# Performance work log

Hardware: AMD Instinct MI355X
Metric: run time of the kernel (lower is better)

Reference implementation:

```python
import jax, jax.numpy as jnp
import numpy as np

B, C, H, W = 8, 256, 32, 32
DK, HEADS = 64, 4
DQ = DK * HEADS            # lambda attention: query dim = dim_key * num_heads
DV = 256 // HEADS          # out_channels // num_heads
EPS = 1e-5
SF = DK ** (-0.25)


def setup_inputs() -> dict:
    key = jax.random.key(0)
    ks = jax.random.split(key, 6)
    inv = 1.0 / np.sqrt(C)
    return {
        "input": jax.random.normal(ks[0], (B, C, H, W), jnp.float32),
        "Wq": jax.random.normal(ks[1], (DQ, C), jnp.float32) * inv,
        "gamma_q": jnp.ones((DQ,), jnp.float32),
        "beta_q": jnp.zeros((DQ,), jnp.float32),
        "Wk": jax.random.normal(ks[2], (DK, C), jnp.float32) * inv,
        "gamma_k": jnp.ones((DK,), jnp.float32),
        "beta_k": jnp.zeros((DK,), jnp.float32),
        "Wv": jax.random.normal(ks[3], (DV, C), jnp.float32) * inv,
        "rpe": jax.random.normal(ks[4], (2 * max(H, W) - 1, 2 * max(H, W) - 1, DK), jnp.float32),
    }


def _bn(x, gamma, beta):
    # BatchNorm2d in training mode: batch stats over (B, H, W), biased variance
    mu = jnp.mean(x, axis=(0, 2, 3), keepdims=True)
    var = jnp.var(x, axis=(0, 2, 3), keepdims=True)
    xn = (x - mu) * jax.lax.rsqrt(var + EPS)
    return xn * gamma[None, :, None, None] + beta[None, :, None, None]


def reference(input, Wq, gamma_q, beta_q, Wk, gamma_k, beta_k, Wv, rpe):
    b, c, h, w = input.shape
    n = h * w
    size = max(h, w)

    # conv1x1 projections (no bias)
    q = _bn(jnp.einsum('oc,bchw->bohw', Wq, input), gamma_q, beta_q)
    k = _bn(jnp.einsum('oc,bchw->bohw', Wk, input), gamma_k, beta_k)
    v = jnp.einsum('oc,bchw->bohw', Wv, input)

    q = q.reshape(b, HEADS, DK, n) * SF          # [b,h,k,n]
    k = k.reshape(b, DK, n) * SF                 # single kv head -> [b,k,n]
    v = v.reshape(b, DV, n)                      # [b,v,n]

    # lambda attention: content lambda
    ks = jax.nn.softmax(k, axis=-1)
    context = jnp.einsum('bkn,bvn->bkv', ks, v)
    out = jnp.einsum('bkv,bhkn->bhvn', context, q)

    # positional lambda via relative position embedding gather
    pos = jnp.arange(size)
    grid = jnp.stack(jnp.meshgrid(pos, pos, indexing='ij'), axis=-1).reshape(-1, 2)  # [n,2]
    rel = grid[None, :] - grid[:, None] + (size - 1)                                 # [n,n,2]
    rg = rpe[rel[..., 0], rel[..., 1]]                                               # [n,n,k]
    pos_context = jnp.einsum('nmk,bvm->bnkv', rg, v)
    out = out + jnp.einsum('bhkn,bnkv->bhvn', q, pos_context)

    return out.reshape(b, -1, h, w)
```

## Files before the change

### kernel.cpp

```cpp
#include <hip/hip_runtime.h>

#define SFC 0.35355339059327373f

typedef __attribute__((ext_vector_type(8))) short short8;
typedef __attribute__((ext_vector_type(16))) float f32x16;
typedef unsigned short ushort_t;

__device__ __forceinline__ float4 ld4(const float* p) { return *reinterpret_cast<const float4*>(p); }
__device__ __forceinline__ void st4(float* p, float4 v) { *reinterpret_cast<float4*>(p) = v; }

union F4 { float4 v; float f[4]; };
union S8 { short8 v; ushort_t u[8]; };

__device__ __forceinline__ ushort_t bfb(float f) {
  union { float f; unsigned u; } a; a.f = f;
  unsigned r = a.u + 0x7FFFu + ((a.u >> 16) & 1u);
  return (ushort_t)(r >> 16);
}

__device__ __forceinline__ void gl16(const void* g, void* l) {
  __builtin_amdgcn_global_load_lds(
      (const __attribute__((address_space(1))) unsigned int*)g,
      (__attribute__((address_space(3))) unsigned int*)l, 16, 0, 0);
}

__global__ __launch_bounds__(256) void k_prep(
    const float* __restrict__ rpe, const float* __restrict__ wq,
    const float* __restrict__ wk, const float* __restrict__ wv,
    const float* __restrict__ x, ushort_t* __restrict__ RPEB2,
    ushort_t* __restrict__ WB, ushort_t* __restrict__ XBT)
{
  const int bx = blockIdx.x, t = threadIdx.x;
  if (bx < 63) {
    const int di = bx;
#pragma unroll
    for (int it = 0; it < 2; ++it) {
      const int slot = t + it * 256;
      const int tkc = slot >> 6;
      const int l = slot & 63, lnp = l & 31, hip = l >> 5;
      const int dj = (tkc >> 2) * 32 + lnp;
      const int k = (tkc & 3) * 16 + hip * 8;
      S8 o;
      if (dj < 63) {
        const float* s = rpe + (size_t)di * 4032 + dj * 64 + k;
        float4 a = ld4(s), b = ld4(s + 4);
        o.u[0] = bfb(a.x); o.u[1] = bfb(a.y); o.u[2] = bfb(a.z); o.u[3] = bfb(a.w);
        o.u[4] = bfb(b.x); o.u[5] = bfb(b.y); o.u[6] = bfb(b.z); o.u[7] = bfb(b.w);
      } else {
#pragma unroll
        for (int i = 0; i < 8; ++i) o.u[i] = 0;
      }
      *(short8*)(RPEB2 + (size_t)di * 4096 + tkc * 512 + l * 8) = o.v;
    }
  } else if (bx < 111) {
    const int cc = (bx - 63) * 256 + t;
    const int o = cc >> 5, k8 = (cc & 31) * 8;
    const float* src = (o < 256) ? (wq + o * 256)
                      : (o < 320) ? (wk + (o - 256) * 256)
                                  : (wv + (o - 320) * 256);
    float4 a = ld4(src + k8), b = ld4(src + k8 + 4);
    S8 s;
    s.u[0] = bfb(a.x); s.u[1] = bfb(a.y); s.u[2] = bfb(a.z); s.u[3] = bfb(a.w);
    s.u[4] = bfb(b.x); s.u[5] = bfb(b.y); s.u[6] = bfb(b.z); s.u[7] = bfb(b.w);
    *(short8*)(WB + (size_t)o * 256 + k8) = s.v;
  } else {
    const int id = (bx - 111) * 256 + t;
    const int ng = id & 8191, c8 = id >> 13;
    const int bb = ng >> 10, nn = ng & 1023;
    const float* src = x + (size_t)bb * 262144 + (size_t)(c8 * 8) * 1024 + nn;
    S8 s;
#pragma unroll
    for (int j = 0; j < 8; ++j) s.u[j] = bfb(src[(size_t)j * 1024]);
    *(short8*)(XBT + (size_t)ng * 256 + c8 * 8) = s.v;
  }
}

__global__ __launch_bounds__(256) void k_projm(
    const ushort_t* __restrict__ WB, const ushort_t* __restrict__ XBT,
    float* __restrict__ P, ushort_t* __restrict__ VB2,
    float* __restrict__ PSUM, float* __restrict__ PSQ)
{
  __shared__ ushort_t At[64 * 72];
  __shared__ ushort_t Bt[128 * 72];
  const int t = threadIdx.x;
  const int bm = blockIdx.x, bn = blockIdx.y;
  const int o0 = bm * 64, col0 = bn * 128;
  const int w = t >> 6, l = t & 63, ln = l & 31, hi = l >> 5;
  const int wm = w & 1, wn = w >> 1;

  f32x16 acc0, acc1;
#pragma unroll
  for (int i = 0; i < 16; ++i) { acc0[i] = 0.f; acc1[i] = 0.f; }

  for (int k0 = 0; k0 < 256; k0 += 64) {
    __syncthreads();
#pragma unroll
    for (int i = 0; i < 2; ++i) {
      const int c = t + i * 256, row = c >> 3, k8 = (c & 7) * 8;
      *(short8*)(At + row * 72 + k8) =
          *(const short8*)(WB + (size_t)(o0 + row) * 256 + k0 + k8);
    }
#pragma unroll
    for (int i = 0; i < 4; ++i) {
      const int c = t + i * 256, row = c >> 3, k8 = (c & 7) * 8;
      *(short8*)(Bt + row * 72 + k8) =
          *(const short8*)(XBT + (size_t)(col0 + row) * 256 + k0 + k8);
    }
    __syncthreads();
    const ushort_t* ka  = At + (wm * 32 + ln) * 72 + hi * 8;
    const ushort_t* kb0 = Bt + (wn * 64 + ln) * 72 + hi * 8;
    const ushort_t* kb1 = Bt + (wn * 64 + 32 + ln) * 72 + hi * 8;
#pragma unroll
    for (int kc = 0; kc < 4; ++kc) {
      short8 a = *(const short8*)(ka + kc * 16);
      acc0 = __builtin_amdgcn_mfma_f32_32x32x16_bf16(a, *(const short8*)(kb0 + kc * 16), acc0, 0, 0, 0);
      acc1 = __builtin_amdgcn_mfma_f32_32x32x16_bf16(a, *(const short8*)(kb1 + kc * 16), acc1, 0, 0, 0);
    }
  }

#pragma unroll
  for (int r = 0; r < 16; ++r) {
    const int o = o0 + wm * 32 + (r & 3) + 8 * (r >> 2) + 4 * hi;
    float* dst = P + (size_t)o * 8192 + col0 + wn * 64 + ln;
    dst[0]  = acc0[r];
    dst[32] = acc1[r];
  }
  if (bm == 5) {
    const int b2 = bn >> 3;
    const int n0 = (bn & 7) * 128 + wn * 64 + ln;
#pragma unroll
    for (int r = 0; r < 16; ++r) {
      const int v = wm * 32 + (r & 3) + 8 * (r >> 2) + 4 * hi;
#pragma unroll
      for (int half = 0; half < 2; ++half) {
        const int n = n0 + half * 32;
        const int i2 = n >> 5, j2 = n & 31;
        const float val = half ? acc1[r] : acc0[r];
        VB2[(((size_t)(b2 * 32 + i2) * 2 + wm) * 2 + (j2 >> 4)) * 512
            + ((v & 31) + 32 * ((j2 >> 3) & 1)) * 8 + (j2 & 7)] = bfb(val);
      }
    }
  } else {
#pragma unroll
    for (int r = 0; r < 16; ++r) {
      float s1 = acc0[r] + acc1[r];
      float s2 = acc0[r] * acc0[r] + acc1[r] * acc1[r];
#pragma unroll
      for (int off = 1; off < 32; off <<= 1) {
        s1 += __shfl_xor(s1, off, 64);
        s2 += __shfl_xor(s2, off, 64);
      }
      if (ln == 0) {
        const int o = o0 + wm * 32 + (r & 3) + 8 * (r >> 2) + 4 * hi;
        PSUM[o * 128 + bn * 2 + wn] = s1;
        PSQ [o * 128 + bn * 2 + wn] = s2;
      }
    }
  }
}

__global__ __launch_bounds__(128) void k_bnfin(
    const float* __restrict__ PSUM, const float* __restrict__ PSQ,
    const float* __restrict__ gq, const float* __restrict__ bq,
    const float* __restrict__ gk, const float* __restrict__ bk,
    float* __restrict__ scale, float* __restrict__ shift)
{
  const int ch = blockIdx.x, t = threadIdx.x;
  float s1 = PSUM[ch * 128 + t];
  float s2 = PSQ[ch * 128 + t];
#pragma unroll
  for (int off = 1; off < 64; off <<= 1) {
    s1 += __shfl_xor(s1, off, 64);
    s2 += __shfl_xor(s2, off, 64);
  }
  __shared__ float red[4];
  if ((t & 63) == 0) { red[t >> 6] = s1; red[2 + (t >> 6)] = s2; }
  __syncthreads();
  if (t == 0) {
    s1 = red[0] + red[1];
    s2 = red[2] + red[3];
    const float mu = s1 * (1.0f / 8192.0f);
    const float var = s2 * (1.0f / 8192.0f) - mu * mu;
    const float rsig = rsqrtf(var + 1e-5f);
    float g, be;
    if (ch < 256) { g = gq[ch]; be = bq[ch]; }
    else          { g = gk[ch - 256]; be = bk[ch - 256]; }
    const float sc = rsig * g * SFC;
    scale[ch] = sc;
    shift[ch] = be * SFC - mu * sc;
  }
}

__global__ __launch_bounds__(256) void k_softmax(
    const float* __restrict__ P, const float* __restrict__ scale,
    const float* __restrict__ shift, ushort_t* __restrict__ KSB)
{
  const int b = blockIdx.x >> 6, kc = blockIdx.x & 63;
  const int ch = 256 + kc;
  const float sc = scale[ch], sh = shift[ch];
  const float4* row = (const float4*)(P + (size_t)ch * 8192 + b * 1024);
  float4 v = row[threadIdx.x];
  float y0 = v.x * sc + sh, y1 = v.y * sc + sh;
  float y2 = v.z * sc + sh, y3 = v.w * sc + sh;
  float m = fmaxf(fmaxf(y0, y1), fmaxf(y2, y3));
#pragma unroll
  for (int off = 32; off; off >>= 1) m = fmaxf(m, __shfl_xor(m, off, 64));
  __shared__ float red[8];
  const int w = threadIdx.x >> 6, lane = threadIdx.x & 63;
  if (lane == 0) red[w] = m;
  __syncthreads();
  m = fmaxf(fmaxf(red[0], red[1]), fmaxf(red[2], red[3]));
  const float e0 = __expf(y0 - m), e1 = __expf(y1 - m);
  const float e2 = __expf(y2 - m), e3 = __expf(y3 - m);
  float su = e0 + e1 + e2 + e3;
#pragma unroll
  for (int off = 32; off; off >>= 1) su += __shfl_xor(su, off, 64);
  if (lane == 0) red[4 + w] = su;
  __syncthreads();
  const float inv = 1.0f / (red[4] + red[5] + red[6] + red[7]);
  ushort4 u;
  u.x = bfb(e0 * inv); u.y = bfb(e1 * inv);
  u.z = bfb(e2 * inv); u.w = bfb(e3 * inv);
  ((ushort4*)(KSB + (size_t)(b * 64 + kc) * 1024))[threadIdx.x] = u;
}

__global__ __launch_bounds__(256) void k_ctxm(
    const ushort_t* __restrict__ KSB, const ushort_t* __restrict__ VB2,
    ushort_t* __restrict__ CTXB)
{
  __shared__ ushort_t KT[2][64 * 72];
  const int b = blockIdx.x, t = threadIdx.x;
  const int w = t >> 6, l = t & 63, ln = l & 31, hi = l >> 5;
  const int a = w & 1, bt = w >> 1;

  auto stageK = [&](int ch, int buf) {
    const int n0 = ch * 64;
#pragma unroll
    for (int it = 0; it < 2; ++it) {
      const int idx = t + it * 256;
      const int row = idx >> 3, seg = idx & 7;
      *(short8*)(&KT[buf][row * 72 + seg * 8]) =
          *(const short8*)(KSB + (size_t)(b * 64 + row) * 1024 + n0 + seg * 8);
    }
  };

  f32x16 acc;
#pragma unroll
  for (int i = 0; i < 16; ++i) acc[i] = 0.f;

  stageK(0, 0);
  for (int ch = 0; ch < 16; ++ch) {
    const int cur = ch & 1;
    __syncthreads();
    if (ch + 1 < 16) stageK(ch + 1, cur ^ 1);
    const ushort_t* ka = &KT[cur][(a * 32 + ln) * 72 + hi * 8];
#pragma unroll
    for (int cc = 0; cc < 4; ++cc) {
      const int i2 = ch * 2 + (cc >> 1), c = cc & 1;
      short8 bf = *(const short8*)(VB2 +
          (((size_t)(b * 32 + i2) * 2 + bt) * 2 + c) * 512 + l * 8);
      acc = __builtin_amdgcn_mfma_f32_32x32x16_bf16(
          *(const short8*)(ka + cc * 16), bf, acc, 0, 0, 0);
    }
  }
#pragma unroll
  for (int r = 0; r < 16; ++r) {
    const int kc = a * 32 + (r & 3) + 8 * (r >> 2) + 4 * hi;
    CTXB[(size_t)b * 4608 + (bt * 32 + ln) * 72 + kc] = bfb(acc[r]);
  }
}

extern __shared__ char ldsc[];

__global__ __launch_bounds__(512) void k_pos(
    const float* __restrict__ P, const ushort_t* __restrict__ RPEB2,
    const ushort_t* __restrict__ VB2, const float* __restrict__ scale,
    const float* __restrict__ shift, const ushort_t* __restrict__ CTXB,
    float* __restrict__ out)
{
  float* qst = (float*)ldsc;
  ushort_t* SlB = (ushort_t*)(ldsc + 33792);
  char* CtxL = ldsc + 54272;

  const int t = threadIdx.x;
  const int b = blockIdx.x >> 5, i1 = blockIdx.x & 31;
  const int w = t >> 6, l = t & 63, ln = l & 31, hi = l >> 5;
  const int m = w & 3, g = w >> 2;

  {
    const char* cs = (const char*)CTXB + (size_t)b * 9216;
    gl16(cs + w * 1024 + l * 16, CtxL + w * 1024 + l * 16);
    if (w == 0) gl16(cs + 8192 + l * 16, CtxL + 8192 + l * 16);
  }

  const ushort_t* rbase = RPEB2 + (size_t)(g * 16 - i1 + 31) * 4096;
  const ushort_t* vbase = VB2 + (size_t)(b * 32 + g * 16) * 2048;

  short8 rA[8], rB[8];
#pragma unroll
  for (int f = 0; f < 8; ++f) rA[f] = *(const short8*)(rbase + f * 512 + l * 8);

  {
    const int j1 = t & 31, c0 = (t >> 5) * 16;
    const float* src = P + (size_t)b * 1024 + i1 * 32 + j1;
#pragma unroll
    for (int i = 0; i < 16; ++i) {
      const int ch = c0 + i;
      qst[ch * 33 + j1] = src[(size_t)ch * 8192] * scale[ch] + shift[ch];
    }
  }
  __syncthreads();

  short8 qf[4];
#pragma unroll
  for (int kc = 0; kc < 4; ++kc) {
    S8 s;
#pragma unroll
    for (int i = 0; i < 8; ++i)
      s.u[i] = bfb(qst[(m * 64 + kc * 16 + hi * 8 + i) * 33 + ln]);
    qf[kc] = s.v;
  }

  f32x16 sv0, sv1;
#pragma unroll
  for (int i = 0; i < 16; ++i) { sv0[i] = 0.f; sv1[i] = 0.f; }

  ushort_t* sm = SlB + w * 1280;

  auto body = [&](int s, const short8* R) {
    const ushort_t* vp = vbase + (size_t)s * 2048 + l * 8;
    short8 v00 = *(const short8*)(vp);
    short8 v01 = *(const short8*)(vp + 512);
    short8 v10 = *(const short8*)(vp + 1024);
    short8 v11 = *(const short8*)(vp + 1536);
    f32x16 t0, t1;
#pragma unroll
    for (int i = 0; i < 16; ++i) { t0[i] = 0.f; t1[i] = 0.f; }
#pragma unroll
    for (int kc = 0; kc < 4; ++kc) {
      t0 = __builtin_amdgcn_mfma_f32_32x32x16_bf16(qf[kc], R[kc],     t0, 0, 0, 0);
      t1 = __builtin_amdgcn_mfma_f32_32x32x16_bf16(qf[kc], R[4 + kc], t1, 0, 0, 0);
    }
#pragma unroll
    for (int r = 0; r < 16; ++r) {
      const int j1 = (r & 3) + 8 * (r >> 2) + 4 * hi;
      const int j2a = ln + j1 - 31;
      const int j2b = 32 + ln + j1 - 31;
      if ((unsigned)j2a < 32u) sm[j1 * 40 + j2a] = bfb(t0[r]);
      if ((unsigned)j2b < 32u) sm[j1 * 40 + j2b] = bfb(t1[r]);
    }
    const ushort_t* sa = sm + ln * 40 + hi * 8;
    short8 sA0 = *(const short8*)(sa);
    short8 sA1 = *(const short8*)(sa + 16);
    sv0 = __builtin_amdgcn_mfma_f32_32x32x16_bf16(sA0, v00, sv0, 0, 0, 0);
    sv0 = __builtin_amdgcn_mfma_f32_32x32x16_bf16(sA1, v01, sv0, 0, 0, 0);
    sv1 = __builtin_amdgcn_mfma_f32_32x32x16_bf16(sA0, v10, sv1, 0, 0, 0);
    sv1 = __builtin_amdgcn_mfma_f32_32x32x16_bf16(sA1, v11, sv1, 0, 0, 0);
  };

  for (int s = 0; s < 16; s += 2) {
    {
      const ushort_t* rn = rbase + (size_t)(s + 1) * 4096;
#pragma unroll
      for (int f = 0; f < 8; ++f) rB[f] = *(const short8*)(rn + f * 512 + l * 8);
    }
    body(s, rA);
    if (s + 2 < 16) {
      const ushort_t* rn = rbase + (size_t)(s + 2) * 4096;
#pragma unroll
      for (int f = 0; f < 8; ++f) rA[f] = *(const short8*)(rn + f * 512 + l * 8);
    }
    body(s + 1, rB);
  }

  __syncthreads();

  float* out_l = qst;
  if (g == 0) {
    const ushort_t* cb = (const ushort_t*)CtxL;
    const ushort_t* c0 = cb + ln * 72 + hi * 8;
    const ushort_t* c1 = cb + (32 + ln) * 72 + hi * 8;
#pragma unroll
    for (int kc = 0; kc < 4; ++kc) {
      sv0 = __builtin_amdgcn_mfma_f32_32x32x16_bf16(qf[kc], *(const short8*)(c0 + kc * 16), sv0, 0, 0, 0);
      sv1 = __builtin_amdgcn_mfma_f32_32x32x16_bf16(qf[kc], *(const short8*)(c1 + kc * 16), sv1, 0, 0, 0);
    }
  } else {
#pragma unroll
    for (int r = 0; r < 16; ++r) {
      const int j1 = (r & 3) + 8 * (r >> 2) + 4 * hi;
      out_l[(m * 64 + ln) * 33 + j1]      = sv0[r];
      out_l[(m * 64 + 32 + ln) * 33 + j1] = sv1[r];
    }
  }
  __syncthreads();
  if (g == 0) {
#pragma unroll
    for (int r = 0; r < 16; ++r) {
      const int j1 = (r & 3) + 8 * (r >> 2) + 4 * hi;
      out_l[(m * 64 + ln) * 33 + j1]      += sv0[r];
      out_l[(m * 64 + 32 + ln) * 33 + j1] += sv1[r];
    }
  }
  __syncthreads();
  {
    const int ch = t >> 1, jh = (t & 1) * 16;
    float* dst = out + (size_t)b * 262144 + (size_t)ch * 1024 + i1 * 32 + jh;
    const float* srow = out_l + ch * 33 + jh;
#pragma unroll
    for (int gq2 = 0; gq2 < 4; ++gq2)
      st4(dst + gq2 * 4, make_float4(srow[gq2 * 4], srow[gq2 * 4 + 1],
                                     srow[gq2 * 4 + 2], srow[gq2 * 4 + 3]));
  }
}

extern "C" void kernel_launch(void* const* d_in, const int* in_sizes, int n_in,
                              void* d_out, int out_size, void* d_ws, size_t ws_size,
                              hipStream_t stream) {
  const float* x   = (const float*)d_in[0];
  const float* wq  = (const float*)d_in[1];
  const float* gq  = (const float*)d_in[2];
  const float* bq  = (const float*)d_in[3];
  const float* wk  = (const float*)d_in[4];
  const float* gk  = (const float*)d_in[5];
  const float* bk  = (const float*)d_in[6];
  const float* wv  = (const float*)d_in[7];
  const float* rpe = (const float*)d_in[8];
  float* out = (float*)d_out;
  char* W = (char*)d_ws;

  float* P        = (float*)W;
  ushort_t* KSB   = (ushort_t*)(W + 12582912);
  float* PSUM     = (float*)(W + 13631488);
  float* PSQ      = (float*)(W + 13795328);
  float* SCALE    = (float*)(W + 13959168);
  float* SHIFT    = (float*)(W + 13961216);
  ushort_t* CTXB  = (ushort_t*)(W + 13963264);
  ushort_t* RPEB2 = (ushort_t*)(W + 14036992);
  ushort_t* VB2   = (ushort_t*)(W + 14553088);
  ushort_t* WB    = (ushort_t*)(W + 15601664);
  ushort_t* XBT   = (ushort_t*)(W + 15798272);

  k_prep<<<1135, 256, 0, stream>>>(rpe, wq, wk, wv, x, RPEB2, WB, XBT);
  k_projm<<<dim3(6, 64), 256, 0, stream>>>(WB, XBT, P, VB2, PSUM, PSQ);
  k_bnfin<<<320, 128, 0, stream>>>(PSUM, PSQ, gq, bq, gk, bk, SCALE, SHIFT);
  k_softmax<<<512, 256, 0, stream>>>(P, SCALE, SHIFT, KSB);
  k_ctxm<<<8, 256, 0, stream>>>(KSB, VB2, CTXB);

  hipFuncSetAttribute((const void*)k_pos,
                      hipFuncAttributeMaxDynamicSharedMemorySize, 63488);
  k_pos<<<256, 512, 63488, stream>>>(P, RPEB2, VB2, SCALE, SHIFT, CTXB, out);
}
```

Baseline: 62.01 us.

## Store Q as bf16 in MFMA fragment layout, fuse BN finalize into softmax

The projection kernel now writes Q directly as bf16 in the fragment layout k_pos consumes, and keeps only K in fp32. This replaces the full fp32 P buffer with a smaller one and removes the LDS staging and transpose of Q in k_pos. The separate BN-finalize kernel is folded into k_softmax: extra blocks compute the Q scale and shift, while each K block recomputes its own channel stats, which removes one launch. Q is now rounded to bf16 before normalization and rounded again after, which adds a little precision loss.

After: 59.41 us. -4.2%, faster.

```diff
diff --git a/kernel.cpp b/kernel.cpp
--- a/kernel.cpp
+++ b/kernel.cpp
@@ -16,6 +16,9 @@
   union { float f; unsigned u; } a; a.f = f;
   unsigned r = a.u + 0x7FFFu + ((a.u >> 16) & 1u);
   return (ushort_t)(r >> 16);
+}
+__device__ __forceinline__ float bf2f(ushort_t u) {
+  union { unsigned u; float f; } a; a.u = (unsigned)u << 16; return a.f;
 }
 
 __device__ __forceinline__ void gl16(const void* g, void* l) {
@@ -77,8 +80,9 @@
 
 __global__ __launch_bounds__(256) void k_projm(
     const ushort_t* __restrict__ WB, const ushort_t* __restrict__ XBT,
-    float* __restrict__ P, ushort_t* __restrict__ VB2,
-    float* __restrict__ PSUM, float* __restrict__ PSQ)
+    float* __restrict__ Pk, ushort_t* __restrict__ QB,
+    ushort_t* __restrict__ VB2, float* __restrict__ PSUM,
+    float* __restrict__ PSQ)
 {
   __shared__ ushort_t At[64 * 72];
   __shared__ ushort_t Bt[128 * 72];
@@ -118,13 +122,6 @@
     }
   }
 
-#pragma unroll
-  for (int r = 0; r < 16; ++r) {
-    const int o = o0 + wm * 32 + (r & 3) + 8 * (r >> 2) + 4 * hi;
-    float* dst = P + (size_t)o * 8192 + col0 + wn * 64 + ln;
-    dst[0]  = acc0[r];
-    dst[32] = acc1[r];
-  }
   if (bm == 5) {
     const int b2 = bn >> 3;
     const int n0 = (bn & 7) * 128 + wn * 64 + ln;
@@ -141,6 +138,31 @@
       }
     }
   } else {
+    if (bm == 4) {
+#pragma unroll
+      for (int r = 0; r < 16; ++r) {
+        const int o = o0 + wm * 32 + (r & 3) + 8 * (r >> 2) + 4 * hi;
+        float* dst = Pk + (size_t)(o - 256) * 8192 + col0 + wn * 64 + ln;
+        dst[0]  = acc0[r];
+        dst[32] = acc1[r];
+      }
+    } else {
+      const int kcq = 2 * wm;
+#pragma unroll
+      for (int r = 0; r < 16; ++r) {
+        const int kc = kcq + ((r >> 3) & 1);
+        const int lq = ln + 32 * ((r >> 2) & 1);
+        const int iq = (r & 3) + 4 * hi;
+#pragma unroll
+        for (int half = 0; half < 2; ++half) {
+          const int n = col0 + wn * 64 + half * 32 + ln;
+          const int bq_ = n >> 10, i1q = (n >> 5) & 31;
+          const float val = half ? acc1[r] : acc0[r];
+          QB[(((size_t)(bq_ * 32 + i1q) * 4 + bm) * 4 + kc) * 512 + lq * 8 + iq] =
+              bfb(val);
+        }
+      }
+    }
 #pragma unroll
     for (int r = 0; r < 16; ++r) {
       float s1 = acc0[r] + acc1[r];
@@ -159,69 +181,89 @@
   }
 }
 
-__global__ __launch_bounds__(128) void k_bnfin(
-    const float* __restrict__ PSUM, const float* __restrict__ PSQ,
-    const float* __restrict__ gq, const float* __restrict__ bq,
-    const float* __restrict__ gk, const float* __restrict__ bk,
-    float* __restrict__ scale, float* __restrict__ shift)
+__global__ __launch_bounds__(256) void k_softmax(
+    const float* __restrict__ Pk, const float* __restrict__ PSUM,
+    const float* __restrict__ PSQ, const float* __restrict__ gq,
+    const float* __restrict__ bq, const float* __restrict__ gk,
+    const float* __restrict__ bk, float* __restrict__ SCALE,
+    float* __restrict__ SHIFT, ushort_t* __restrict__ KSB)
 {
-  const int ch = blockIdx.x, t = threadIdx.x;
-  float s1 = PSUM[ch * 128 + t];
-  float s2 = PSQ[ch * 128 + t];
-#pragma unroll
-  for (int off = 1; off < 64; off <<= 1) {
-    s1 += __shfl_xor(s1, off, 64);
-    s2 += __shfl_xor(s2, off, 64);
-  }
-  __shared__ float red[4];
-  if ((t & 63) == 0) { red[t >> 6] = s1; red[2 + (t >> 6)] = s2; }
-  __syncthreads();
-  if (t == 0) {
-    s1 = red[0] + red[1];
-    s2 = red[2] + red[3];
-    const float mu = s1 * (1.0f / 8192.0f);
-    const float var = s2 * (1.0f / 8192.0f) - mu * mu;
-    const float rsig = rsqrtf(var + 1e-5f);
-    float g, be;
-    if (ch < 256) { g = gq[ch]; be = bq[ch]; }
-    else          { g = gk[ch - 256]; be = bk[ch - 256]; }
-    const float sc = rsig * g * SFC;
-    scale[ch] = sc;
-    shift[ch] = be * SFC - mu * sc;
-  }
-}
-
-__global__ __launch_bounds__(256) void k_softmax(
-    const float* __restrict__ P, const float* __restrict__ scale,
-    const float* __restrict__ shift, ushort_t* __restrict__ KSB)
-{
+  __shared__ float red[8];
+  __shared__ float scsh[2];
+  const int t = threadIdx.x;
+
+  if (blockIdx.x >= 512) {
+    const int ch = blockIdx.x - 512;
+    float s1 = 0.f, s2 = 0.f;
+    if (t < 128) { s1 = PSUM[ch * 128 + t]; s2 = PSQ[ch * 128 + t]; }
+#pragma unroll
+    for (int off = 1; off < 64; off <<= 1) {
+      s1 += __shfl_xor(s1, off, 64);
+      s2 += __shfl_xor(s2, off, 64);
+    }
+    if ((t & 63) == 0) { red[t >> 6] = s1; red[4 + (t >> 6)] = s2; }
+    __syncthreads();
+    if (t == 0) {
+      s1 = red[0] + red[1] + red[2] + red[3];
+      s2 = red[4] + red[5] + red[6] + red[7];
+      const float mu = s1 * (1.0f / 8192.0f);
+      const float var = s2 * (1.0f / 8192.0f) - mu * mu;
+      const float sc = rsqrtf(var + 1e-5f) * gq[ch] * SFC;
+      SCALE[ch] = sc;
+      SHIFT[ch] = bq[ch] * SFC - mu * sc;
+    }
+    return;
+  }
+
   const int b = blockIdx.x >> 6, kc = blockIdx.x & 63;
-  const int ch = 256 + kc;
-  const float sc = scale[ch], sh = shift[ch];
-  const float4* row = (const float4*)(P + (size_t)ch * 8192 + b * 1024);
-  float4 v = row[threadIdx.x];
+  {
+    const int ch = 256 + kc;
+    float s1 = 0.f, s2 = 0.f;
+    if (t < 128) { s1 = PSUM[ch * 128 + t]; s2 = PSQ[ch * 128 + t]; }
+#pragma unroll
+    for (int off = 1; off < 64; off <<= 1) {
+      s1 += __shfl_xor(s1, off, 64);
+      s2 += __shfl_xor(s2, off, 64);
+    }
+    if ((t & 63) == 0) { red[t >> 6] = s1; red[4 + (t >> 6)] = s2; }
+    __syncthreads();
+    if (t == 0) {
+      s1 = red[0] + red[1] + red[2] + red[3];
+      s2 = red[4] + red[5] + red[6] + red[7];
+      const float mu = s1 * (1.0f / 8192.0f);
+      const float var = s2 * (1.0f / 8192.0f) - mu * mu;
+      const float sc = rsqrtf(var + 1e-5f) * gk[kc] * SFC;
+      scsh[0] = sc;
+      scsh[1] = bk[kc] * SFC - mu * sc;
+    }
+    __syncthreads();
+  }
+  const float sc = scsh[0], sh = scsh[1];
+
+  const float4* row = (const float4*)(Pk + (size_t)kc * 8192 + b * 1024);
+  float4 v = row[t];
   float y0 = v.x * sc + sh, y1 = v.y * sc + sh;
   float y2 = v.z * sc + sh, y3 = v.w * sc + sh;
   float m = fmaxf(fmaxf(y0, y1), fmaxf(y2, y3));
 #pragma unroll
   for (int off = 32; off; off >>= 1) m = fmaxf(m, __shfl_xor(m, off, 64));
-  __shared__ float red[8];
-  const int w = threadIdx.x >> 6, lane = threadIdx.x & 63;
-  if (lane == 0) red[w] = m;
+  __shared__ float red2[8];
+  const int w = t >> 6, lane = t & 63;
+  if (lane == 0) red2[w] = m;
   __syncthreads();
-  m = fmaxf(fmaxf(red[0], red[1]), fmaxf(red[2], red[3]));
+  m = fmaxf(fmaxf(red2[0], red2[1]), fmaxf(red2[2], red2[3]));
   const float e0 = __expf(y0 - m), e1 = __expf(y1 - m);
   const float e2 = __expf(y2 - m), e3 = __expf(y3 - m);
   float su = e0 + e1 + e2 + e3;
 #pragma unroll
   for (int off = 32; off; off >>= 1) su += __shfl_xor(su, off, 64);
-  if (lane == 0) red[4 + w] = su;
+  if (lane == 0) red2[4 + w] = su;
   __syncthreads();
-  const float inv = 1.0f / (red[4] + red[5] + red[6] + red[7]);
+  const float inv = 1.0f / (red2[4] + red2[5] + red2[6] + red2[7]);
   ushort4 u;
   u.x = bfb(e0 * inv); u.y = bfb(e1 * inv);
   u.z = bfb(e2 * inv); u.w = bfb(e3 * inv);
-  ((ushort4*)(KSB + (size_t)(b * 64 + kc) * 1024))[threadIdx.x] = u;
+  ((ushort4*)(KSB + (size_t)(b * 64 + kc) * 1024))[t] = u;
 }
 
 __global__ __launch_bounds__(256) void k_ctxm(
@@ -273,12 +315,12 @@
 extern __shared__ char ldsc[];
 
 __global__ __launch_bounds__(512) void k_pos(
-    const float* __restrict__ P, const ushort_t* __restrict__ RPEB2,
-    const ushort_t* __restrict__ VB2, const float* __restrict__ scale,
-    const float* __restrict__ shift, const ushort_t* __restrict__ CTXB,
+    const ushort_t* __restrict__ QB, const ushort_t* __restrict__ RPEB2,
+    const ushort_t* __restrict__ VB2, const float* __restrict__ SCALE,
+    const float* __restrict__ SHIFT, const ushort_t* __restrict__ CTXB,
     float* __restrict__ out)
 {
-  float* qst = (float*)ldsc;
+  float* out_l = (float*)ldsc;
   ushort_t* SlB = (ushort_t*)(ldsc + 33792);
   char* CtxL = ldsc + 54272;
 
@@ -300,25 +342,26 @@
 #pragma unroll
   for (int f = 0; f < 8; ++f) rA[f] = *(const short8*)(rbase + f * 512 + l * 8);
 
+  short8 qf[4];
   {
-    const int j1 = t & 31, c0 = (t >> 5) * 16;
-    const float* src = P + (size_t)b * 1024 + i1 * 32 + j1;
-#pragma unroll
-    for (int i = 0; i < 16; ++i) {
-      const int ch = c0 + i;
-      qst[ch * 33 + j1] = src[(size_t)ch * 8192] * scale[ch] + shift[ch];
-    }
-  }
-  __syncthreads();
-
-  short8 qf[4];
-#pragma unroll
-  for (int kc = 0; kc < 4; ++kc) {
-    S8 s;
-#pragma unroll
-    for (int i = 0; i < 8; ++i)
-      s.u[i] = bfb(qst[(m * 64 + kc * 16 + hi * 8 + i) * 33 + ln]);
-    qf[kc] = s.v;
+    const ushort_t* qb = QB + (((size_t)(b * 32 + i1) * 4 + m) * 4) * 512 + l * 8;
+#pragma unroll
+    for (int kc = 0; kc < 4; ++kc) {
+      S8 raw; raw.v = *(const short8*)(qb + kc * 512);
+      const int chb = m * 64 + kc * 16 + hi * 8;
+      F4 s0, s1, h0, h1;
+      s0.v = ld4(SCALE + chb); s1.v = ld4(SCALE + chb + 4);
+      h0.v = ld4(SHIFT + chb); h1.v = ld4(SHIFT + chb + 4);
+      S8 o;
+#pragma unroll
+      for (int i = 0; i < 8; ++i) {
+        const float f = bf2f(raw.u[i]);
+        const float scv = (i < 4) ? s0.f[i] : s1.f[i - 4];
+        const float shv = (i < 4) ? h0.f[i] : h1.f[i - 4];
+        o.u[i] = bfb(f * scv + shv);
+      }
+      qf[kc] = o.v;
+    }
   }
 
   f32x16 sv0, sv1;
@@ -375,7 +418,6 @@
 
   __syncthreads();
 
-  float* out_l = qst;
   if (g == 0) {
     const ushort_t* cb = (const ushort_t*)CtxL;
     const ushort_t* c0 = cb + ln * 72 + hi * 8;
@@ -429,25 +471,25 @@
   float* out = (float*)d_out;
   char* W = (char*)d_ws;
 
-  float* P        = (float*)W;
-  ushort_t* KSB   = (ushort_t*)(W + 12582912);
-  float* PSUM     = (float*)(W + 13631488);
-  float* PSQ      = (float*)(W + 13795328);
-  float* SCALE    = (float*)(W + 13959168);
-  float* SHIFT    = (float*)(W + 13961216);
-  ushort_t* CTXB  = (ushort_t*)(W + 13963264);
-  ushort_t* RPEB2 = (ushort_t*)(W + 14036992);
-  ushort_t* VB2   = (ushort_t*)(W + 14553088);
-  ushort_t* WB    = (ushort_t*)(W + 15601664);
-  ushort_t* XBT   = (ushort_t*)(W + 15798272);
+  float* Pk       = (float*)W;
+  ushort_t* QB    = (ushort_t*)(W + 2097152);
+  ushort_t* KSB   = (ushort_t*)(W + 6291456);
+  float* PSUM     = (float*)(W + 7340032);
+  float* PSQ      = (float*)(W + 7503872);
+  float* SCALE    = (float*)(W + 7667712);
+  float* SHIFT    = (float*)(W + 7669760);
+  ushort_t* CTXB  = (ushort_t*)(W + 7671808);
+  ushort_t* RPEB2 = (ushort_t*)(W + 7745536);
+  ushort_t* VB2   = (ushort_t*)(W + 8261632);
+  ushort_t* WB    = (ushort_t*)(W + 9310208);
+  ushort_t* XBT   = (ushort_t*)(W + 9506816);
 
   k_prep<<<1135, 256, 0, stream>>>(rpe, wq, wk, wv, x, RPEB2, WB, XBT);
-  k_projm<<<dim3(6, 64), 256, 0, stream>>>(WB, XBT, P, VB2, PSUM, PSQ);
-  k_bnfin<<<320, 128, 0, stream>>>(PSUM, PSQ, gq, bq, gk, bk, SCALE, SHIFT);
-  k_softmax<<<512, 256, 0, stream>>>(P, SCALE, SHIFT, KSB);
+  k_projm<<<dim3(6, 64), 256, 0, stream>>>(WB, XBT, Pk, QB, VB2, PSUM, PSQ);
+  k_softmax<<<768, 256, 0, stream>>>(Pk, PSUM, PSQ, gq, bq, gk, bk, SCALE, SHIFT, KSB);
   k_ctxm<<<8, 256, 0, stream>>>(KSB, VB2, CTXB);
 
   hipFuncSetAttribute((const void*)k_pos,
                       hipFuncAttributeMaxDynamicSharedMemorySize, 63488);
-  k_pos<<<256, 512, 63488, stream>>>(P, RPEB2, VB2, SCALE, SHIFT, CTXB, out);
-}
+  k_pos<<<256, 512, 63488, stream>>>(QB, RPEB2, VB2, SCALE, SHIFT, CTXB, out);
+}
```
